# Performance work log

Hardware: AMD Instinct MI355X
Metric: run time of the kernel (lower is better)

## Reference

```python
import jax, jax.numpy as jnp
import numpy as np

K_N = 20          # neighbors (init kwarg k_n)
EPS = 1e-5        # BN / InstanceNorm eps (torch default)


def _conv1x1(x, w, b):
    # x: [B,C,N,K], w: [O,C], b: [O]
    return jnp.einsum('bcnk,oc->bonk', x, w) + b[None, :, None, None]


def _bn(x, g, b):
    # training-mode BatchNorm2d: stats over (B,N,K)
    mean = x.mean(axis=(0, 2, 3), keepdims=True)
    var = x.var(axis=(0, 2, 3), keepdims=True)
    return (x - mean) * jax.lax.rsqrt(var + EPS) * g[None, :, None, None] + b[None, :, None, None]


def _inorm(x):
    # InstanceNorm2d (affine=False): stats over (N,K) per (b,c)
    mean = x.mean(axis=(2, 3), keepdims=True)
    var = x.var(axis=(2, 3), keepdims=True)
    return (x - mean) * jax.lax.rsqrt(var + EPS)


def _knn(x, k):
    # x: [B,C,N] -> idx [B,N,k] of nearest neighbors (excluding self)
    sq = jnp.sum(x * x, axis=1)                                   # [B,N]
    neg_d = 2.0 * jnp.einsum('bcn,bcm->bnm', x, x) - sq[:, :, None] - sq[:, None, :]
    _, idx = jax.lax.top_k(neg_d, k + 1)
    return idx[:, :, 1:]


def _res_block(x, w1, b1, g1, be1, w2, b2, g2, be2):
    # pre=False: residual branch is identity
    out = jax.nn.relu(_bn(_inorm(_conv1x1(x, w1, b1)), g1, be1))
    out = _bn(_inorm(_conv1x1(out, w2, b2)), g2, be2)
    return jax.nn.relu(out + x)


def _forward(data, conv0_w, conv0_b, bn0_g, bn0_b, lin_w, lin_b,
             res_w1, res_b1, res_g1, res_be1, res_w2, res_b2, res_g2, res_be2):
    B, C, N = data.shape
    # graph_feature: degree feature from normalized affinity matrix
    nrm = jnp.linalg.norm(data, axis=1, keepdims=True) + 1e-5
    o = data / nrm
    A = jnp.einsum('bcn,bcm->bnm', o, o)                          # [B,N,N]
    D = (jnp.sum(A, axis=1, keepdims=True) - 1.0) / N             # [B,1,N] (subtract eye diag)
    feat = jnp.concatenate([data, jax.nn.relu(jnp.tanh(D))], axis=1)  # [B,129,N]

    idx = _knn(feat, K_N)                                         # [B,N,k]
    xt = jnp.transpose(feat, (0, 2, 1))                           # [B,N,129]
    gathered = jax.vmap(lambda xb, ib: xb[ib])(xt, idx)           # [B,N,k,129]
    center = xt[:, :, None, :]
    edge = jnp.concatenate([jnp.broadcast_to(center, gathered.shape),
                            center - gathered], axis=3)           # [B,N,k,258]
    edge = jnp.transpose(edge, (0, 3, 1, 2))                      # [B,258,N,k]

    out = jax.nn.relu(_bn(_conv1x1(edge, conv0_w, conv0_b), bn0_g, bn0_b))
    out = jnp.max(out, axis=3, keepdims=True)                     # max_pool2d (1,k) -> [B,128,N,1]
    for i in range(4):
        out = _res_block(out, res_w1[i], res_b1[i], res_g1[i], res_be1[i],
                         res_w2[i], res_b2[i], res_g2[i], res_be2[i])
    logit = _conv1x1(out, lin_w, lin_b)                           # [B,1,N,1]
    return logit.reshape(logit.shape[0], -1)                      # [B,N]


def setup_inputs() -> dict:
    B, C, N = 8, 128, 2048
    key = jax.random.key(0)
    ks = jax.random.split(key, 10)
    s = 0.05
    return {
        'data': jax.random.normal(ks[0], (B, C, N), dtype=jnp.float32),
        'x': jax.random.normal(ks[1], (B, C, N), dtype=jnp.float32),  # unused by module
        'conv0_w': jax.random.normal(ks[2], (128, 258), dtype=jnp.float32) * s,
        'conv0_b': jnp.zeros((128,), dtype=jnp.float32),
        'bn0_g': jnp.ones((128,), dtype=jnp.float32),
        'bn0_b': jnp.zeros((128,), dtype=jnp.float32),
        'lin_w': jax.random.normal(ks[3], (1, 128), dtype=jnp.float32) * s,
        'lin_b': jnp.zeros((1,), dtype=jnp.float32),
        'res_w1': jax.random.normal(ks[4], (4, 128, 128), dtype=jnp.float32) * s,
        'res_b1': jnp.zeros((4, 128), dtype=jnp.float32),
        'res_g1': jnp.ones((4, 128), dtype=jnp.float32),
        'res_be1': jnp.zeros((4, 128), dtype=jnp.float32),
        'res_w2': jax.random.normal(ks[5], (4, 128, 128), dtype=jnp.float32) * s,
        'res_b2': jnp.zeros((4, 128), dtype=jnp.float32),
        'res_g2': jnp.ones((4, 128), dtype=jnp.float32),
        'res_be2': jnp.zeros((4, 128), dtype=jnp.float32),
    }


def reference(data, x, conv0_w, conv0_b, bn0_g, bn0_b, lin_w, lin_b,
              res_w1, res_b1, res_g1, res_be1, res_w2, res_b2, res_g2, res_be2):
    # x is accepted but unused, matching the torch module
    return _forward(data, conv0_w, conv0_b, bn0_g, bn0_b, lin_w, lin_b,
                    res_w1, res_b1, res_g1, res_be1, res_w2, res_b2, res_g2, res_be2)
```

## Files before the change

kernel.cpp:

```cpp
#include <hip/hip_runtime.h>
#include <math.h>
#include <float.h>

#define NB 8
#define NC 128
#define NN 2048
#define KNN 20
#define CF 129
#define CFP 144
#define EPSV 1e-5f

#define S_OFF      0
#define BN0S_OFF   1024
#define RESST_OFF  1280
#define NRM_OFF    17664
#define ZERO_CNT   34048
#define SQN_OFF    34048
#define WCAT_OFF   50432
#define BN0AFF_OFF 87296
#define RESAFF_OFF 87552
#define FEAT_OFF   103936
#define PQ_OFF     2463232
#define X_OFF      6657536
#define SLOT_SZ    2097152
#define IDX_OFF    12948992
#define G_OFF      13276672
#define WS_FLOATS  46831104
#define MMN_OFF    (X_OFF + SLOT_SZ)
#define MMX_OFF    (X_OFF + 2 * SLOT_SZ)

__launch_bounds__(256)
__global__ void k1a_sq(const float* __restrict__ data, float* __restrict__ ws) {
    int b = blockIdx.y;
    int n = blockIdx.x * 256 + threadIdx.x;
    int c0 = blockIdx.z * 32;
    const float* dp = data + (size_t)b * NC * NN + (size_t)c0 * NN + n;
    float acc = 0.f;
#pragma unroll
    for (int c = 0; c < 32; ++c) { float v = dp[(size_t)c * NN]; acc = fmaf(v, v, acc); }
    atomicAdd(&ws[NRM_OFF + b * NN + n], acc);
}

__launch_bounds__(256)
__global__ void k1s_colsum(const float* __restrict__ data, float* __restrict__ ws) {
    int b = blockIdx.y;
    int c0 = blockIdx.x * 16;
    int tid = threadIdx.x, w = tid >> 6, lane = tid & 63;
    __shared__ float Linv[NN];
    for (int r = tid; r < NN; r += 256)
        Linv[r] = 1.f / (sqrtf(ws[NRM_OFF + b * NN + r]) + 1e-5f);
    __syncthreads();
#pragma unroll
    for (int i = 0; i < 4; ++i) {
        int c = c0 + w * 4 + i;
        const float* dp = data + (size_t)b * NC * NN + (size_t)c * NN;
        float acc = 0.f;
        for (int n = lane; n < NN; n += 64) acc = fmaf(dp[n], Linv[n], acc);
        for (int off = 32; off; off >>= 1) acc += __shfl_down(acc, off);
        if (lane == 0) ws[S_OFF + b * NC + c] = acc;
    }
}

__launch_bounds__(256)
__global__ void k2_feat(const float* __restrict__ data, float* __restrict__ ws) {
    int b = blockIdx.y;
    int n0 = blockIdx.x * 64;
    int tid = threadIdx.x;
    __shared__ float Sb[NC];
    __shared__ __align__(16) float fT[64][CFP];
    __shared__ float redD[4][64], redQ[4][64];
    if (tid < NC) Sb[tid] = ws[S_OFF + b * NC + tid];
    __syncthreads();
    int nn = tid & 63, cg = tid >> 6;
    float dotp = 0.f, sq = 0.f;
    const float* dp = data + (size_t)b * NC * NN + n0 + nn;
    for (int c = cg; c < NC; c += 4) {
        float v = dp[(size_t)c * NN];
        fT[nn][c] = v;
        dotp += Sb[c] * v;
        sq += v * v;
    }
    redD[cg][nn] = dotp; redQ[cg][nn] = sq;
    __syncthreads();
    if (tid < 64) {
        float dt = redD[0][tid] + redD[1][tid] + redD[2][tid] + redD[3][tid];
        float sv = redQ[0][tid] + redQ[1][tid] + redQ[2][tid] + redQ[3][tid];
        float nrm = sqrtf(ws[NRM_OFF + b * NN + n0 + tid]) + 1e-5f;
        float D = (dt / nrm - 1.f) * (1.f / (float)NN);
        float f1 = tanhf(D); if (f1 < 0.f) f1 = 0.f;
        fT[tid][NC] = f1;
        for (int c = NC + 1; c < CFP; ++c) fT[tid][c] = 0.f;
        ws[SQN_OFF + b * NN + n0 + tid] = sv + f1 * f1;
    }
    __syncthreads();
    float* out = ws + FEAT_OFF + (size_t)(b * NN + n0) * CFP;
    for (int i = tid; i < 64 * CFP; i += 256) out[i] = ((float*)fT)[i];
}

__launch_bounds__(256)
__global__ void k4_wcat(const float* __restrict__ w, float* __restrict__ ws) {
    int i = blockIdx.x * 256 + threadIdx.x;
    int o = i / CFP, c = i % CFP;
    float v = 0.f;
    if (c < CF) {
        if (o < 128) v = w[o * 258 + c] + w[o * 258 + CF + c];
        else         v = w[(o - 128) * 258 + CF + c];
    }
    ws[WCAT_OFF + i] = v;
}

__launch_bounds__(256)
__global__ void k3_gram(float* __restrict__ ws) {
    __shared__ __align__(16) float As[8][128];
    __shared__ __align__(16) float Bs[8][128];
    int tid = threadIdx.x;
    int b = blockIdx.z;
    int m0 = blockIdx.x * 128, n0 = blockIdx.y * 128;
    const float* F = ws + FEAT_OFF + (size_t)b * NN * CFP;
    float acc[8][8];
#pragma unroll
    for (int i = 0; i < 8; ++i)
#pragma unroll
        for (int j = 0; j < 8; ++j) acc[i][j] = 0.f;
    int rr = tid >> 1, cq = tid & 1;
    int tx = tid & 15, ty = tid >> 4;
    for (int kc = 0; kc < CFP; kc += 8) {
        float4 av = *(const float4*)&F[(size_t)(n0 + rr) * CFP + kc + cq * 4];
        float4 bv = *(const float4*)&F[(size_t)(m0 + rr) * CFP + kc + cq * 4];
        __syncthreads();
        As[cq*4+0][rr] = av.x; As[cq*4+1][rr] = av.y; As[cq*4+2][rr] = av.z; As[cq*4+3][rr] = av.w;
        Bs[cq*4+0][rr] = bv.x; Bs[cq*4+1][rr] = bv.y; Bs[cq*4+2][rr] = bv.z; Bs[cq*4+3][rr] = bv.w;
        __syncthreads();
#pragma unroll
        for (int kk = 0; kk < 8; ++kk) {
            float a[8], bb[8];
            *(float4*)&a[0]  = *(const float4*)&As[kk][ty * 8];
            *(float4*)&a[4]  = *(const float4*)&As[kk][ty * 8 + 4];
            *(float4*)&bb[0] = *(const float4*)&Bs[kk][tx * 4];
            *(float4*)&bb[4] = *(const float4*)&Bs[kk][64 + tx * 4];
#pragma unroll
            for (int i = 0; i < 8; ++i)
#pragma unroll
                for (int j = 0; j < 8; ++j) acc[i][j] = fmaf(a[i], bb[j], acc[i][j]);
        }
    }
    float sqv[8];
#pragma unroll
    for (int j = 0; j < 4; ++j) {
        sqv[j]     = ws[SQN_OFF + b * NN + m0 + tx * 4 + j];
        sqv[4 + j] = ws[SQN_OFF + b * NN + m0 + 64 + tx * 4 + j];
    }
    float* G = ws + G_OFF + (size_t)b * NN * NN;
#pragma unroll
    for (int i = 0; i < 8; ++i) {
        int row = n0 + ty * 8 + i;
        float4 o1, o2;
        o1.x = 2.f*acc[i][0]-sqv[0]; o1.y = 2.f*acc[i][1]-sqv[1];
        o1.z = 2.f*acc[i][2]-sqv[2]; o1.w = 2.f*acc[i][3]-sqv[3];
        o2.x = 2.f*acc[i][4]-sqv[4]; o2.y = 2.f*acc[i][5]-sqv[5];
        o2.z = 2.f*acc[i][6]-sqv[6]; o2.w = 2.f*acc[i][7]-sqv[7];
        *(float4*)&G[(size_t)row * NN + m0 + tx * 4]      = o1;
        *(float4*)&G[(size_t)row * NN + m0 + 64 + tx * 4] = o2;
    }
}

__launch_bounds__(256)
__global__ void ksel(float* __restrict__ ws) {
    int wid = threadIdx.x >> 6, lane = threadIdx.x & 63;
    int r = blockIdx.x * 4 + wid;
    const float* row = ws + G_OFF + (size_t)r * NN;
    float v[32];
#pragma unroll
    for (int i = 0; i < 32; ++i) v[i] = row[lane + (i << 6)];
    float b1v = -FLT_MAX, b2v = -FLT_MAX;
    int b1i = 0, b2i = 0;
#pragma unroll
    for (int i = 0; i < 32; ++i) {
        float x = v[i];
        if (x > b1v)      { b2v = b1v; b2i = b1i; b1v = x; b1i = i; }
        else if (x > b2v) { b2v = x; b2i = i; }
    }
    unsigned int mask = 0u;
    bool has2 = true;
    int* out = (int*)(ws + IDX_OFF) + (size_t)r * KNN;
    for (int k = 0; k < 21; ++k) {
        float M = b1v;
#pragma unroll
        for (int off = 1; off < 64; off <<= 1) M = fmaxf(M, __shfl_xor(M, off));
        unsigned long long tied = __ballot(b1v == M);
        int mm;
        if (__popcll(tied) > 1) {
            int cand = (b1v == M) ? ((b1i << 6) | lane) : 0x7FFFFFFF;
#pragma unroll
            for (int off = 1; off < 64; off <<= 1) {
                int oc = __shfl_xor(cand, off);
                cand = oc < cand ? oc : cand;
            }
            mm = cand;
        } else {
            int l = __ffsll(tied) - 1;
            mm = (__shfl(b1i, l) << 6) | l;
        }
        if (k > 0 && lane == 0) out[k - 1] = mm;
        if (lane == (mm & 63)) {
            mask |= 1u << b1i;
            if (has2) { b1v = b2v; b1i = b2i; has2 = false; }
            else {
                b1v = -FLT_MAX; b2v = -FLT_MAX; b1i = 0; b2i = 0;
#pragma unroll
                for (int i = 0; i < 32; ++i) {
                    float x = (mask & (1u << i)) ? -FLT_MAX : v[i];
                    if (x > b1v)      { b2v = b1v; b2i = b1i; b1v = x; b1i = i; }
                    else if (x > b2v) { b2v = x; b2i = i; }
                }
                has2 = true;
            }
        }
    }
}

__launch_bounds__(256)
__global__ void k5_pq(float* __restrict__ ws) {
    __shared__ __align__(16) float As[16][64];
    __shared__ __align__(16) float Bs[16][64];
    int tid = threadIdx.x;
    int m0 = blockIdx.x * 64, o0 = blockIdx.y * 64;
    int rr = tid >> 2, cq = tid & 3;
    int tx = tid & 15, ty = tid >> 4;
    float acc[4][4];
#pragma unroll
    for (int i = 0; i < 4; ++i)
#pragma unroll
        for (int j = 0; j < 4; ++j) acc[i][j] = 0.f;
    const float* F  = ws + FEAT_OFF;
    const float* Wc = ws + WCAT_OFF;
    for (int kc = 0; kc < CFP; kc += 16) {
        float4 av = *(const float4*)&F [(size_t)(m0 + rr) * CFP + kc + cq * 4];
        float4 bv = *(const float4*)&Wc[(size_t)(o0 + rr) * CFP + kc + cq * 4];
        __syncthreads();
        As[cq*4+0][rr]=av.x; As[cq*4+1][rr]=av.y; As[cq*4+2][rr]=av.z; As[cq*4+3][rr]=av.w;
        Bs[cq*4+0][rr]=bv.x; Bs[cq*4+1][rr]=bv.y; Bs[cq*4+2][rr]=bv.z; Bs[cq*4+3][rr]=bv.w;
        __syncthreads();
#pragma unroll
        for (int kk = 0; kk < 16; ++kk) {
            float a[4], bb[4];
            *(float4*)&a[0]  = *(const float4*)&As[kk][ty * 4];
            *(float4*)&bb[0] = *(const float4*)&Bs[kk][tx * 4];
#pragma unroll
            for (int i = 0; i < 4; ++i)
#pragma unroll
                for (int j = 0; j < 4; ++j) acc[i][j] = fmaf(a[i], bb[j], acc[i][j]);
        }
    }
#pragma unroll
    for (int i = 0; i < 4; ++i) {
        float4 o;
        o.x = acc[i][0]; o.y = acc[i][1]; o.z = acc[i][2]; o.w = acc[i][3];
        *(float4*)&ws[PQ_OFF + (size_t)(m0 + ty * 4 + i) * 256 + o0 + tx * 4] = o;
    }
}

__launch_bounds__(256)
__global__ void k6_bn0stats(float* __restrict__ ws) {
    int tid = threadIdx.x;
    int o = tid & 127, h = tid >> 7;
    int m0 = blockIdx.x * 64;
    const float* PQ = ws + PQ_OFF;
    const int* idx = (const int*)(ws + IDX_OFF);
    float* MMn = ws + MMN_OFF;
    float* MMx = ws + MMX_OFF;
    __shared__ float red[2][128];
    float s = 0.f, q = 0.f;
    for (int p = h; p < 64; p += 2) {
        int m = m0 + p;
        int bb = m >> 11;
        float pv = PQ[(size_t)m * 256 + o];
        const int* ip = idx + (size_t)m * KNN;
        float mn = FLT_MAX, mx = -FLT_MAX;
        for (int k = 0; k < KNN; ++k) {
            int j = ip[k];
            float val = pv - PQ[(size_t)(bb * NN + j) * 256 + 128 + o];
            s += val; q += val * val;
            mn = fminf(mn, val); mx = fmaxf(mx, val);
        }
        MMn[(size_t)m * NC + o] = mn;
        MMx[(size_t)m * NC + o] = mx;
    }
    red[h][o] = s; __syncthreads();
    if (tid < 128) atomicAdd(&ws[BN0S_OFF + tid], red[0][tid] + red[1][tid]);
    __syncthreads();
    red[h][o] = q; __syncthreads();
    if (tid < 128) atomicAdd(&ws[BN0S_OFF + 128 + tid], red[0][tid] + red[1][tid]);
}

__global__ void k7_bn0fin(float* __restrict__ ws, const float* __restrict__ g,
                          const float* __restrict__ be) {
    int o = threadIdx.x;
    float cnt = 1.f / (float)(NB * NN * KNN);
    float sum = ws[BN0S_OFF + o], ssq = ws[BN0S_OFF + 128 + o];
    float m = sum * cnt;
    float v = ssq * cnt - m * m; if (v < 0.f) v = 0.f;
    float sc = g[o] * rsqrtf(v + EPSV);
    float sh = be[o] - m * sc;
    ws[BN0AFF_OFF + o] = sc; ws[BN0AFF_OFF + 128 + o] = sh;
}

__launch_bounds__(256)
__global__ void k8_apply(float* __restrict__ ws) {
    int e = blockIdx.x * 256 + threadIdx.x;
    int fi = e * 4;
    int o = fi & 127;
    const float* MMn = ws + MMN_OFF;
    const float* MMx = ws + MMX_OFF;
    float4 mn = *(const float4*)&MMn[fi];
    float4 mx = *(const float4*)&MMx[fi];
    const float* aff = ws + BN0AFF_OFF;
    float4 r;
    float sc, sh;
    sc = aff[o];     sh = aff[128 + o];     r.x = fmaxf(fmaf(sc > 0.f ? mx.x : mn.x, sc, sh), 0.f);
    sc = aff[o + 1]; sh = aff[128 + o + 1]; r.y = fmaxf(fmaf(sc > 0.f ? mx.y : mn.y, sc, sh), 0.f);
    sc = aff[o + 2]; sh = aff[128 + o + 2]; r.z = fmaxf(fmaf(sc > 0.f ? mx.z : mn.z, sc, sh), 0.f);
    sc = aff[o + 3]; sh = aff[128 + o + 3]; r.w = fmaxf(fmaf(sc > 0.f ? mx.w : mn.w, sc, sh), 0.f);
    *(float4*)&ws[X_OFF + fi] = r;
}

__launch_bounds__(256)
__global__ void k9f_conv(const float* __restrict__ x, const float* __restrict__ w,
                         float* __restrict__ y, float* __restrict__ stats,
                         const float* __restrict__ aff) {
    __shared__ __align__(16) float As[16][64];
    __shared__ __align__(16) float Bs[16][64];
    __shared__ float red[16][64];
    int tid = threadIdx.x;
    int m0 = blockIdx.x * 64, o0 = blockIdx.y * 64;
    int rr = tid >> 2, cq = tid & 3;
    int tx = tid & 15, ty = tid >> 4;
    int bA = (m0 + rr) >> 11;
    float acc[4][4];
#pragma unroll
    for (int i = 0; i < 4; ++i)
#pragma unroll
        for (int j = 0; j < 4; ++j) acc[i][j] = 0.f;
    for (int kc = 0; kc < NC; kc += 16) {
        float4 av = *(const float4*)&x[(size_t)(m0 + rr) * NC + kc + cq * 4];
        if (aff) {
            int c = kc + cq * 4;
            float4 sc4 = *(const float4*)&aff[bA * 128 + c];
            float4 sh4 = *(const float4*)&aff[1024 + bA * 128 + c];
            av.x = fmaxf(fmaf(av.x, sc4.x, sh4.x), 0.f);
            av.y = fmaxf(fmaf(av.y, sc4.y, sh4.y), 0.f);
            av.z = fmaxf(fmaf(av.z, sc4.z, sh4.z), 0.f);
            av.w = fmaxf(fmaf(av.w, sc4.w, sh4.w), 0.f);
        }
        float4 bv = *(const float4*)&w[(size_t)(o0 + rr) * NC + kc + cq * 4];
        __syncthreads();
        As[cq*4+0][rr]=av.x; As[cq*4+1][rr]=av.y; As[cq*4+2][rr]=av.z; As[cq*4+3][rr]=av.w;
        Bs[cq*4+0][rr]=bv.x; Bs[cq*4+1][rr]=bv.y; Bs[cq*4+2][rr]=bv.z; Bs[cq*4+3][rr]=bv.w;
        __syncthreads();
#pragma unroll
        for (int kk = 0; kk < 16; ++kk) {
            float a[4], bb[4];
            *(float4*)&a[0]  = *(const float4*)&As[kk][ty * 4];
            *(float4*)&bb[0] = *(const float4*)&Bs[kk][tx * 4];
#pragma unroll
            for (int i = 0; i < 4; ++i)
#pragma unroll
                for (int j = 0; j < 4; ++j) acc[i][j] = fmaf(a[i], bb[j], acc[i][j]);
        }
    }
#pragma unroll
    for (int i = 0; i < 4; ++i) {
        float4 o;
        o.x = acc[i][0]; o.y = acc[i][1]; o.z = acc[i][2]; o.w = acc[i][3];
        *(float4*)&y[(size_t)(m0 + ty * 4 + i) * NC + o0 + tx * 4] = o;
    }
    int b = m0 >> 11;
    float s[4], q[4];
#pragma unroll
    for (int j = 0; j < 4; ++j) {
        s[j] = acc[0][j] + acc[1][j] + acc[2][j] + acc[3][j];
        q[j] = acc[0][j]*acc[0][j] + acc[1][j]*acc[1][j] + acc[2][j]*acc[2][j] + acc[3][j]*acc[3][j];
    }
    *(float4*)&red[ty][tx * 4] = make_float4(s[0], s[1], s[2], s[3]);
    __syncthreads();
    if (tid < 64) {
        float t = 0.f;
#pragma unroll
        for (int g2 = 0; g2 < 16; ++g2) t += red[g2][tid];
        atomicAdd(&stats[b * NC + o0 + tid], t);
    }
    __syncthreads();
    *(float4*)&red[ty][tx * 4] = make_float4(q[0], q[1], q[2], q[3]);
    __syncthreads();
    if (tid < 64) {
        float t = 0.f;
#pragma unroll
        for (int g2 = 0; g2 < 16; ++g2) t += red[g2][tid];
        atomicAdd(&stats[1024 + b * NC + o0 + tid], t);
    }
}

__launch_bounds__(1024)
__global__ void k10_fin(float* __restrict__ ws, int L, const float* __restrict__ g,
                        const float* __restrict__ be) {
    __shared__ float vv[1024];
    __shared__ float rsbn[128];
    int tid = threadIdx.x;
    const float* st = ws + RESST_OFF + L * 2048;
    float sum = st[tid], ssq = st[1024 + tid];
    float m = sum * (1.f / (float)NN);
    float v = ssq * (1.f / (float)NN) - m * m; if (v < 0.f) v = 0.f;
    float r = rsqrtf(v + EPSV);
    vv[tid] = v / (v + EPSV);
    __syncthreads();
    if (tid < 128) {
        float a = 0.f;
        for (int bb = 0; bb < NB; ++bb) a += vv[bb * 128 + tid];
        rsbn[tid] = rsqrtf(a * (1.f / (float)NB) + EPSV);
    }
    __syncthreads();
    int o = tid & 127;
    float sc = r * rsbn[o] * g[o];
    float sh = be[o] - m * sc;
    float* aff = ws + RESAFF_OFF + L * 2048;
    aff[tid] = sc; aff[1024 + tid] = sh;
}

__launch_bounds__(256)
__global__ void k11_norm(const float* __restrict__ y, float* __restrict__ out,
                         const float* __restrict__ aff, const float* __restrict__ xin) {
    int e = blockIdx.x * 256 + threadIdx.x;
    int fi = e * 4;
    int o = fi & 127;
    int b = fi >> 18;
    const float* sc = aff + b * 128;
    const float* sh = aff + 1024 + b * 128;
    float4 yv = *(const float4*)&y[fi];
    float4 r;
    r.x = yv.x * sc[o]     + sh[o];
    r.y = yv.y * sc[o + 1] + sh[o + 1];
    r.z = yv.z * sc[o + 2] + sh[o + 2];
    r.w = yv.w * sc[o + 3] + sh[o + 3];
    if (xin) {
        float4 xv = *(const float4*)&xin[fi];
        r.x += xv.x; r.y += xv.y; r.z += xv.z; r.w += xv.w;
    }
    r.x = fmaxf(r.x, 0.f); r.y = fmaxf(r.y, 0.f);
    r.z = fmaxf(r.z, 0.f); r.w = fmaxf(r.w, 0.f);
    *(float4*)&out[fi] = r;
}

__launch_bounds__(256)
__global__ void k12_logit(const float* __restrict__ xs, const float* __restrict__ lw,
                          const float* __restrict__ lb, float* __restrict__ out) {
    __shared__ float w[128];
    int tid = threadIdx.x;
    if (tid < 128) w[tid] = lw[tid];
    __syncthreads();
    int m = blockIdx.x * 256 + tid;
    const float* xp = xs + (size_t)m * NC;
    float acc = lb[0];
    for (int c = 0; c < NC; c += 4) {
        float4 xv = *(const float4*)&xp[c];
        acc += xv.x * w[c] + xv.y * w[c + 1] + xv.z * w[c + 2] + xv.w * w[c + 3];
    }
    out[m] = acc;
}

extern "C" void kernel_launch(void* const* d_in, const int* in_sizes, int n_in,
                              void* d_out, int out_size, void* d_ws, size_t ws_size,
                              hipStream_t stream) {
    if (ws_size < (size_t)WS_FLOATS * 4) return;
    const float* data    = (const float*)d_in[0];
    const float* conv0_w = (const float*)d_in[2];
    const float* bn0_g   = (const float*)d_in[4];
    const float* bn0_b   = (const float*)d_in[5];
    const float* lin_w   = (const float*)d_in[6];
    const float* lin_b   = (const float*)d_in[7];
    const float* res_w1  = (const float*)d_in[8];
    const float* res_g1  = (const float*)d_in[10];
    const float* res_be1 = (const float*)d_in[11];
    const float* res_w2  = (const float*)d_in[12];
    const float* res_g2  = (const float*)d_in[14];
    const float* res_be2 = (const float*)d_in[15];
    float* ws  = (float*)d_ws;
    float* out = (float*)d_out;

    hipMemsetAsync(d_ws, 0, ZERO_CNT * sizeof(float), stream);
    k1a_sq<<<dim3(8, 8, 4), 256, 0, stream>>>(data, ws);
    k1s_colsum<<<dim3(8, 8), 256, 0, stream>>>(data, ws);
    k2_feat<<<dim3(32, 8), 256, 0, stream>>>(data, ws);
    k4_wcat<<<144, 256, 0, stream>>>(conv0_w, ws);
    k3_gram<<<dim3(16, 16, 8), 256, 0, stream>>>(ws);
    ksel<<<4096, 256, 0, stream>>>(ws);
    k5_pq<<<dim3(256, 4), 256, 0, stream>>>(ws);
    k6_bn0stats<<<256, 256, 0, stream>>>(ws);
    k7_bn0fin<<<1, 128, 0, stream>>>(ws, bn0_g, bn0_b);
    k8_apply<<<2048, 256, 0, stream>>>(ws);

    float* slot0 = ws + X_OFF;
    float* slot1 = ws + X_OFF + SLOT_SZ;
    float* slot2 = ws + X_OFF + 2 * SLOT_SZ;
    for (int i = 0; i < 4; ++i) {
        int L = 2 * i, L2 = 2 * i + 1;
        k9f_conv<<<dim3(256, 2), 256, 0, stream>>>(slot0, res_w1 + i * 16384, slot1,
                                                   ws + RESST_OFF + L * 2048, nullptr);
        k10_fin<<<1, 1024, 0, stream>>>(ws, L, res_g1 + i * 128, res_be1 + i * 128);
        k9f_conv<<<dim3(256, 2), 256, 0, stream>>>(slot1, res_w2 + i * 16384, slot2,
                                                   ws + RESST_OFF + L2 * 2048,
                                                   ws + RESAFF_OFF + L * 2048);
        k10_fin<<<1, 1024, 0, stream>>>(ws, L2, res_g2 + i * 128, res_be2 + i * 128);
        k11_norm<<<2048, 256, 0, stream>>>(slot2, slot0, ws + RESAFF_OFF + L2 * 2048, slot0);
    }
    k12_logit<<<64, 256, 0, stream>>>(slot0, lin_w, lin_b, out);
}
```

Measured before the change: 461.1 us.

## Fuse residual norm into conv prologue, enlarge gram tile, fold BN0 finalize

The per-block residual normalize kernel is removed. Its affine, residual add and ReLU now run inside the next conv's input load, with the first column-block writing out the new residual, and the last one is fused into the logit kernel. The BN0 finalize kernel is folded into the apply kernel. The gram kernel tile grows to 256x128 with 16x8 accumulators per thread, and the bn0stats grid uses 4x more blocks. Together these remove several launches and full-tensor read/write passes, at the cost of higher register pressure in the gram kernel and an extra workspace buffer.

```diff
diff --git a/kernel.cpp b/kernel.cpp
--- a/kernel.cpp
+++ b/kernel.cpp
@@ -17,7 +17,6 @@
 #define ZERO_CNT   34048
 #define SQN_OFF    34048
 #define WCAT_OFF   50432
-#define BN0AFF_OFF 87296
 #define RESAFF_OFF 87552
 #define FEAT_OFF   103936
 #define PQ_OFF     2463232
@@ -25,7 +24,8 @@
 #define SLOT_SZ    2097152
 #define IDX_OFF    12948992
 #define G_OFF      13276672
-#define WS_FLOATS  46831104
+#define XB_OFF     46831104
+#define WS_FLOATS  48928256
 #define MMN_OFF    (X_OFF + SLOT_SZ)
 #define MMX_OFF    (X_OFF + 2 * SLOT_SZ)
 
@@ -109,37 +109,41 @@
     ws[WCAT_OFF + i] = v;
 }
 
-__launch_bounds__(256)
+__launch_bounds__(256, 2)
 __global__ void k3_gram(float* __restrict__ ws) {
-    __shared__ __align__(16) float As[8][128];
+    __shared__ __align__(16) float As[8][256];
     __shared__ __align__(16) float Bs[8][128];
     int tid = threadIdx.x;
     int b = blockIdx.z;
-    int m0 = blockIdx.x * 128, n0 = blockIdx.y * 128;
+    int m0 = blockIdx.x * 128, n0 = blockIdx.y * 256;
     const float* F = ws + FEAT_OFF + (size_t)b * NN * CFP;
-    float acc[8][8];
-#pragma unroll
-    for (int i = 0; i < 8; ++i)
+    float acc[16][8];
+#pragma unroll
+    for (int i = 0; i < 16; ++i)
 #pragma unroll
         for (int j = 0; j < 8; ++j) acc[i][j] = 0.f;
     int rr = tid >> 1, cq = tid & 1;
     int tx = tid & 15, ty = tid >> 4;
     for (int kc = 0; kc < CFP; kc += 8) {
-        float4 av = *(const float4*)&F[(size_t)(n0 + rr) * CFP + kc + cq * 4];
+        float4 a0 = *(const float4*)&F[(size_t)(n0 + tid) * CFP + kc];
+        float4 a1 = *(const float4*)&F[(size_t)(n0 + tid) * CFP + kc + 4];
         float4 bv = *(const float4*)&F[(size_t)(m0 + rr) * CFP + kc + cq * 4];
         __syncthreads();
-        As[cq*4+0][rr] = av.x; As[cq*4+1][rr] = av.y; As[cq*4+2][rr] = av.z; As[cq*4+3][rr] = av.w;
+        As[0][tid] = a0.x; As[1][tid] = a0.y; As[2][tid] = a0.z; As[3][tid] = a0.w;
+        As[4][tid] = a1.x; As[5][tid] = a1.y; As[6][tid] = a1.z; As[7][tid] = a1.w;
         Bs[cq*4+0][rr] = bv.x; Bs[cq*4+1][rr] = bv.y; Bs[cq*4+2][rr] = bv.z; Bs[cq*4+3][rr] = bv.w;
         __syncthreads();
 #pragma unroll
         for (int kk = 0; kk < 8; ++kk) {
-            float a[8], bb[8];
-            *(float4*)&a[0]  = *(const float4*)&As[kk][ty * 8];
-            *(float4*)&a[4]  = *(const float4*)&As[kk][ty * 8 + 4];
+            float a[16], bb[8];
+            *(float4*)&a[0]  = *(const float4*)&As[kk][ty * 16];
+            *(float4*)&a[4]  = *(const float4*)&As[kk][ty * 16 + 4];
+            *(float4*)&a[8]  = *(const float4*)&As[kk][ty * 16 + 8];
+            *(float4*)&a[12] = *(const float4*)&As[kk][ty * 16 + 12];
             *(float4*)&bb[0] = *(const float4*)&Bs[kk][tx * 4];
             *(float4*)&bb[4] = *(const float4*)&Bs[kk][64 + tx * 4];
 #pragma unroll
-            for (int i = 0; i < 8; ++i)
+            for (int i = 0; i < 16; ++i)
 #pragma unroll
                 for (int j = 0; j < 8; ++j) acc[i][j] = fmaf(a[i], bb[j], acc[i][j]);
         }
@@ -152,8 +156,8 @@
     }
     float* G = ws + G_OFF + (size_t)b * NN * NN;
 #pragma unroll
-    for (int i = 0; i < 8; ++i) {
-        int row = n0 + ty * 8 + i;
+    for (int i = 0; i < 16; ++i) {
+        int row = n0 + ty * 16 + i;
         float4 o1, o2;
         o1.x = 2.f*acc[i][0]-sqv[0]; o1.y = 2.f*acc[i][1]-sqv[1];
         o1.z = 2.f*acc[i][2]-sqv[2]; o1.w = 2.f*acc[i][3]-sqv[3];
@@ -264,14 +268,14 @@
 __global__ void k6_bn0stats(float* __restrict__ ws) {
     int tid = threadIdx.x;
     int o = tid & 127, h = tid >> 7;
-    int m0 = blockIdx.x * 64;
+    int m0 = blockIdx.x * 16;
     const float* PQ = ws + PQ_OFF;
     const int* idx = (const int*)(ws + IDX_OFF);
     float* MMn = ws + MMN_OFF;
     float* MMx = ws + MMX_OFF;
     __shared__ float red[2][128];
     float s = 0.f, q = 0.f;
-    for (int p = h; p < 64; p += 2) {
+    for (int p = h; p < 16; p += 2) {
         int m = m0 + p;
         int bb = m >> 11;
         float pv = PQ[(size_t)m * 256 + o];
@@ -293,41 +297,36 @@
     if (tid < 128) atomicAdd(&ws[BN0S_OFF + 128 + tid], red[0][tid] + red[1][tid]);
 }
 
-__global__ void k7_bn0fin(float* __restrict__ ws, const float* __restrict__ g,
-                          const float* __restrict__ be) {
-    int o = threadIdx.x;
-    float cnt = 1.f / (float)(NB * NN * KNN);
-    float sum = ws[BN0S_OFF + o], ssq = ws[BN0S_OFF + 128 + o];
-    float m = sum * cnt;
-    float v = ssq * cnt - m * m; if (v < 0.f) v = 0.f;
-    float sc = g[o] * rsqrtf(v + EPSV);
-    float sh = be[o] - m * sc;
-    ws[BN0AFF_OFF + o] = sc; ws[BN0AFF_OFF + 128 + o] = sh;
-}
-
-__launch_bounds__(256)
-__global__ void k8_apply(float* __restrict__ ws) {
+__launch_bounds__(256)
+__global__ void k8_apply(float* __restrict__ ws, const float* __restrict__ g,
+                         const float* __restrict__ be) {
     int e = blockIdx.x * 256 + threadIdx.x;
     int fi = e * 4;
     int o = fi & 127;
-    const float* MMn = ws + MMN_OFF;
-    const float* MMx = ws + MMX_OFF;
-    float4 mn = *(const float4*)&MMn[fi];
-    float4 mx = *(const float4*)&MMx[fi];
-    const float* aff = ws + BN0AFF_OFF;
+    const float cnt = 1.f / (float)(NB * NN * KNN);
+    float4 sum4 = *(const float4*)&ws[BN0S_OFF + o];
+    float4 ssq4 = *(const float4*)&ws[BN0S_OFF + 128 + o];
+    float4 g4   = *(const float4*)&g[o];
+    float4 be4  = *(const float4*)&be[o];
+    float4 mn = *(const float4*)&ws[MMN_OFF + fi];
+    float4 mx = *(const float4*)&ws[MMX_OFF + fi];
     float4 r;
-    float sc, sh;
-    sc = aff[o];     sh = aff[128 + o];     r.x = fmaxf(fmaf(sc > 0.f ? mx.x : mn.x, sc, sh), 0.f);
-    sc = aff[o + 1]; sh = aff[128 + o + 1]; r.y = fmaxf(fmaf(sc > 0.f ? mx.y : mn.y, sc, sh), 0.f);
-    sc = aff[o + 2]; sh = aff[128 + o + 2]; r.z = fmaxf(fmaf(sc > 0.f ? mx.z : mn.z, sc, sh), 0.f);
-    sc = aff[o + 3]; sh = aff[128 + o + 3]; r.w = fmaxf(fmaf(sc > 0.f ? mx.w : mn.w, sc, sh), 0.f);
+#define BN0_DO(comp) { \
+    float m_ = sum4.comp * cnt; \
+    float v_ = ssq4.comp * cnt - m_ * m_; if (v_ < 0.f) v_ = 0.f; \
+    float sc_ = g4.comp * rsqrtf(v_ + EPSV); \
+    float sh_ = be4.comp - m_ * sc_; \
+    r.comp = fmaxf(fmaf(sc_ > 0.f ? mx.comp : mn.comp, sc_, sh_), 0.f); }
+    BN0_DO(x) BN0_DO(y) BN0_DO(z) BN0_DO(w)
+#undef BN0_DO
     *(float4*)&ws[X_OFF + fi] = r;
 }
 
 __launch_bounds__(256)
 __global__ void k9f_conv(const float* __restrict__ x, const float* __restrict__ w,
                          float* __restrict__ y, float* __restrict__ stats,
-                         const float* __restrict__ aff) {
+                         const float* __restrict__ aff, const float* __restrict__ xin,
+                         float* __restrict__ xw) {
     __shared__ __align__(16) float As[16][64];
     __shared__ __align__(16) float Bs[16][64];
     __shared__ float red[16][64];
@@ -347,10 +346,18 @@
             int c = kc + cq * 4;
             float4 sc4 = *(const float4*)&aff[bA * 128 + c];
             float4 sh4 = *(const float4*)&aff[1024 + bA * 128 + c];
-            av.x = fmaxf(fmaf(av.x, sc4.x, sh4.x), 0.f);
-            av.y = fmaxf(fmaf(av.y, sc4.y, sh4.y), 0.f);
-            av.z = fmaxf(fmaf(av.z, sc4.z, sh4.z), 0.f);
-            av.w = fmaxf(fmaf(av.w, sc4.w, sh4.w), 0.f);
+            av.x = fmaf(av.x, sc4.x, sh4.x);
+            av.y = fmaf(av.y, sc4.y, sh4.y);
+            av.z = fmaf(av.z, sc4.z, sh4.z);
+            av.w = fmaf(av.w, sc4.w, sh4.w);
+            if (xin) {
+                float4 xv = *(const float4*)&xin[(size_t)(m0 + rr) * NC + kc + cq * 4];
+                av.x += xv.x; av.y += xv.y; av.z += xv.z; av.w += xv.w;
+            }
+            av.x = fmaxf(av.x, 0.f); av.y = fmaxf(av.y, 0.f);
+            av.z = fmaxf(av.z, 0.f); av.w = fmaxf(av.w, 0.f);
+            if (xw && blockIdx.y == 0)
+                *(float4*)&xw[(size_t)(m0 + rr) * NC + kc + cq * 4] = av;
         }
         float4 bv = *(const float4*)&w[(size_t)(o0 + rr) * NC + kc + cq * 4];
         __syncthreads();
@@ -427,42 +434,28 @@
 }
 
 __launch_bounds__(256)
-__global__ void k11_norm(const float* __restrict__ y, float* __restrict__ out,
-                         const float* __restrict__ aff, const float* __restrict__ xin) {
-    int e = blockIdx.x * 256 + threadIdx.x;
-    int fi = e * 4;
-    int o = fi & 127;
-    int b = fi >> 18;
+__global__ void k12_logit(const float* __restrict__ y2, const float* __restrict__ xin,
+                          const float* __restrict__ aff, const float* __restrict__ lw,
+                          const float* __restrict__ lb, float* __restrict__ out) {
+    __shared__ float w[128];
+    int tid = threadIdx.x;
+    if (tid < 128) w[tid] = lw[tid];
+    __syncthreads();
+    int m = blockIdx.x * 256 + tid;
+    int b = m >> 11;
+    const float* yp = y2 + (size_t)m * NC;
+    const float* xp = xin + (size_t)m * NC;
     const float* sc = aff + b * 128;
     const float* sh = aff + 1024 + b * 128;
-    float4 yv = *(const float4*)&y[fi];
-    float4 r;
-    r.x = yv.x * sc[o]     + sh[o];
-    r.y = yv.y * sc[o + 1] + sh[o + 1];
-    r.z = yv.z * sc[o + 2] + sh[o + 2];
-    r.w = yv.w * sc[o + 3] + sh[o + 3];
-    if (xin) {
-        float4 xv = *(const float4*)&xin[fi];
-        r.x += xv.x; r.y += xv.y; r.z += xv.z; r.w += xv.w;
-    }
-    r.x = fmaxf(r.x, 0.f); r.y = fmaxf(r.y, 0.f);
-    r.z = fmaxf(r.z, 0.f); r.w = fmaxf(r.w, 0.f);
-    *(float4*)&out[fi] = r;
-}
-
-__launch_bounds__(256)
-__global__ void k12_logit(const float* __restrict__ xs, const float* __restrict__ lw,
-                          const float* __restrict__ lb, float* __restrict__ out) {
-    __shared__ float w[128];
-    int tid = threadIdx.x;
-    if (tid < 128) w[tid] = lw[tid];
-    __syncthreads();
-    int m = blockIdx.x * 256 + tid;
-    const float* xp = xs + (size_t)m * NC;
     float acc = lb[0];
     for (int c = 0; c < NC; c += 4) {
+        float4 yv = *(const float4*)&yp[c];
         float4 xv = *(const float4*)&xp[c];
-        acc += xv.x * w[c] + xv.y * w[c + 1] + xv.z * w[c + 2] + xv.w * w[c + 3];
+        float v0 = fmaxf(fmaf(yv.x, sc[c],     sh[c])     + xv.x, 0.f);
+        float v1 = fmaxf(fmaf(yv.y, sc[c + 1], sh[c + 1]) + xv.y, 0.f);
+        float v2 = fmaxf(fmaf(yv.z, sc[c + 2], sh[c + 2]) + xv.z, 0.f);
+        float v3 = fmaxf(fmaf(yv.w, sc[c + 3], sh[c + 3]) + xv.w, 0.f);
+        acc += v0 * w[c] + v1 * w[c + 1] + v2 * w[c + 2] + v3 * w[c + 3];
     }
     out[m] = acc;
 }
@@ -491,26 +484,34 @@
     k1s_colsum<<<dim3(8, 8), 256, 0, stream>>>(data, ws);
     k2_feat<<<dim3(32, 8), 256, 0, stream>>>(data, ws);
     k4_wcat<<<144, 256, 0, stream>>>(conv0_w, ws);
-    k3_gram<<<dim3(16, 16, 8), 256, 0, stream>>>(ws);
+    k3_gram<<<dim3(16, 8, 8), 256, 0, stream>>>(ws);
     ksel<<<4096, 256, 0, stream>>>(ws);
     k5_pq<<<dim3(256, 4), 256, 0, stream>>>(ws);
-    k6_bn0stats<<<256, 256, 0, stream>>>(ws);
-    k7_bn0fin<<<1, 128, 0, stream>>>(ws, bn0_g, bn0_b);
-    k8_apply<<<2048, 256, 0, stream>>>(ws);
-
-    float* slot0 = ws + X_OFF;
-    float* slot1 = ws + X_OFF + SLOT_SZ;
-    float* slot2 = ws + X_OFF + 2 * SLOT_SZ;
-    for (int i = 0; i < 4; ++i) {
+    k6_bn0stats<<<1024, 256, 0, stream>>>(ws);
+    k8_apply<<<2048, 256, 0, stream>>>(ws, bn0_g, bn0_b);
+
+    float* XA = ws + X_OFF;
+    float* Y1 = ws + X_OFF + SLOT_SZ;
+    float* Y2 = ws + X_OFF + 2 * SLOT_SZ;
+    float* XB = ws + XB_OFF;
+
+    k9f_conv<<<dim3(256, 2), 256, 0, stream>>>(XA, res_w1, Y1, ws + RESST_OFF, nullptr, nullptr, nullptr);
+    k10_fin<<<1, 1024, 0, stream>>>(ws, 0, res_g1, res_be1);
+    k9f_conv<<<dim3(256, 2), 256, 0, stream>>>(Y1, res_w2, Y2, ws + RESST_OFF + 2048,
+                                               ws + RESAFF_OFF, nullptr, nullptr);
+    k10_fin<<<1, 1024, 0, stream>>>(ws, 1, res_g2, res_be2);
+    float* xcur = XA; float* xnext = XB;
+    for (int i = 1; i < 4; ++i) {
         int L = 2 * i, L2 = 2 * i + 1;
-        k9f_conv<<<dim3(256, 2), 256, 0, stream>>>(slot0, res_w1 + i * 16384, slot1,
-                                                   ws + RESST_OFF + L * 2048, nullptr);
+        k9f_conv<<<dim3(256, 2), 256, 0, stream>>>(Y2, res_w1 + i * 16384, Y1,
+                                                   ws + RESST_OFF + L * 2048,
+                                                   ws + RESAFF_OFF + (L - 1) * 2048, xcur, xnext);
         k10_fin<<<1, 1024, 0, stream>>>(ws, L, res_g1 + i * 128, res_be1 + i * 128);
-        k9f_conv<<<dim3(256, 2), 256, 0, stream>>>(slot1, res_w2 + i * 16384, slot2,
+        k9f_conv<<<dim3(256, 2), 256, 0, stream>>>(Y1, res_w2 + i * 16384, Y2,
                                                    ws + RESST_OFF + L2 * 2048,
-                                                   ws + RESAFF_OFF + L * 2048);
+                                                   ws + RESAFF_OFF + L * 2048, nullptr, nullptr);
         k10_fin<<<1, 1024, 0, stream>>>(ws, L2, res_g2 + i * 128, res_be2 + i * 128);
-        k11_norm<<<2048, 256, 0, stream>>>(slot2, slot0, ws + RESAFF_OFF + L2 * 2048, slot0);
-    }
-    k12_logit<<<64, 256, 0, stream>>>(slot0, lin_w, lin_b, out);
-}
+        float* t = xcur; xcur = xnext; xnext = t;
+    }
+    k12_logit<<<64, 256, 0, stream>>>(Y2, xcur, ws + RESAFF_OFF + 7 * 2048, lin_w, lin_b, out);
+}
```

After: 445.2 us. 3.4% less time.
